# Kernel optimization log

Measured on AMD Instinct MI355X. Metric: run time of the kernel, lower is better.

Reference implementation:

```python
import jax, jax.numpy as jnp
import numpy as np

B, S, E, H = 4, 2048, 1024, 16
D = E // H  # head_dim = 64


def setup_inputs() -> dict:
    key = jax.random.key(0)
    ks = jax.random.split(key, 10)
    scale = 1.0 / np.sqrt(E)
    return {
        "decoder_sequence": jax.random.normal(ks[0], (B, S, E), dtype=jnp.float32),
        # stacked per-head projection weights (math-equivalent to per-head nn.Linear)
        "Wq": jax.random.normal(ks[1], (H, E, D), dtype=jnp.float32) * scale,
        "bq": jnp.zeros((H, D), dtype=jnp.float32),
        "Wk": jax.random.normal(ks[2], (H, E, D), dtype=jnp.float32) * scale,
        "bk": jnp.zeros((H, D), dtype=jnp.float32),
        "Wv": jax.random.normal(ks[3], (H, E, D), dtype=jnp.float32) * scale,
        "bv": jnp.zeros((H, D), dtype=jnp.float32),
        "Wo": jax.random.normal(ks[4], (E, E), dtype=jnp.float32) * scale,
        "bo": jnp.zeros((E,), dtype=jnp.float32),
    }


def reference(decoder_sequence, Wq, bq, Wk, bk, Wv, bv, Wo, bo):
    x = decoder_sequence  # [B,S,E]
    # per-head Q/K/V projections, batched over the head axis
    Q = jnp.einsum('bse,hed->bhsd', x, Wq) + bq[:, None, :]
    K = jnp.einsum('bse,hed->bhsd', x, Wk) + bk[:, None, :]
    V = jnp.einsum('bse,hed->bhsd', x, Wv) + bv[:, None, :]
    # scaled scores with causal mask (upper triangle -> -inf)
    A = jnp.einsum('bhid,bhjd->bhij', Q, K) / jnp.sqrt(jnp.float32(D))
    causal = jnp.tril(jnp.ones((S, S), dtype=bool))  # True where allowed
    A = jnp.where(causal, A, -jnp.inf)
    A = jax.nn.softmax(A, axis=-1)
    Hout = jnp.einsum('bhij,bhjd->bhid', A, V)  # [B,H,S,D]
    # concat heads: [B,S,H*D]
    concat = jnp.transpose(Hout, (0, 2, 1, 3)).reshape(B, S, H * D)
    return concat @ Wo.T + bo
```

## Files before the change

### kernel.cpp

```cpp
#include <hip/hip_runtime.h>
#include <stdint.h>
#include <stddef.h>

typedef __bf16 bf16;
typedef __bf16 bf16x8 __attribute__((ext_vector_type(8)));
typedef __bf16 bf16x4 __attribute__((ext_vector_type(4)));
typedef float  f32x4  __attribute__((ext_vector_type(4)));
typedef float  f32x16 __attribute__((ext_vector_type(16)));
typedef unsigned short ush;
typedef ush ush8 __attribute__((ext_vector_type(8)));
typedef unsigned int uint;

#define B_  4
#define S_  2048
#define E_  1024
#define H_  16
#define D_  64
#define M_  (B_*S_)
#define K_  E_
#define QSCALE 0.18033688011112042f

__device__ __forceinline__ void gload_lds16(const void* g, void* l) {
  __builtin_amdgcn_global_load_lds((const __attribute__((address_space(1))) void*)g,
                                   (__attribute__((address_space(3))) void*)l, 16, 0, 0);
}
__device__ __forceinline__ f32x4 mfma16(bf16x8 a, bf16x8 b, f32x4 c) {
  return __builtin_amdgcn_mfma_f32_16x16x32_bf16(a, b, c, 0, 0, 0);
}
__device__ __forceinline__ f32x16 mfma32(bf16x8 a, bf16x8 b, f32x16 c) {
  return __builtin_amdgcn_mfma_f32_32x32x16_bf16(a, b, c, 0, 0, 0);
}
__device__ __forceinline__ int swz4(int row, int ch) { return ch ^ ((row >> 1) & 3); }
__device__ __forceinline__ uint cvtpk(float lo, float hi) {
  uint r;
  asm("v_cvt_pk_bf16_f32 %0, %1, %2" : "=v"(r) : "v"(lo), "v"(hi));
  return r;
}

__global__ void cast_f32_bf16(const float* __restrict__ src, bf16* __restrict__ dst, int n4) {
  int idx = blockIdx.x * blockDim.x + threadIdx.x;
  int stride = gridDim.x * blockDim.x;
  for (int i = idx; i < n4; i += stride) {
    float4 v = ((const float4*)src)[i];
    union { bf16 b[4]; ushort4 u; } cv;
    cv.b[0] = (bf16)v.x; cv.b[1] = (bf16)v.y; cv.b[2] = (bf16)v.z; cv.b[3] = (bf16)v.w;
    ((ushort4*)dst)[i] = cv.u;
  }
}

__global__ void pack_w_t(const float* __restrict__ Wq, const float* __restrict__ Wk,
                         const float* __restrict__ Wv, bf16* __restrict__ Wp) {
  __shared__ float t[64][65];
  const int tid = threadIdx.x;
  const int wh = blockIdx.y;
  const int which = wh >> 4, h = wh & 15;
  const int e0 = blockIdx.x << 6;
  const float* src = (which == 0) ? Wq : (which == 1 ? Wk : Wv);
  src += (size_t)h * (E_ * D_);
  #pragma unroll
  for (int i = 0; i < 4; ++i) {
    int fi = tid + 256 * i;
    int e = fi >> 4, c = fi & 15;
    float4 v = *(const float4*)(src + (size_t)(e0 + e) * D_ + c * 4);
    t[c * 4 + 0][e] = v.x; t[c * 4 + 1][e] = v.y;
    t[c * 4 + 2][e] = v.z; t[c * 4 + 3][e] = v.w;
  }
  __syncthreads();
  #pragma unroll
  for (int i = 0; i < 2; ++i) {
    int cid = tid + 256 * i;
    int d = cid >> 3, cc = cid & 7;
    ush8 o;
    #pragma unroll
    for (int j = 0; j < 8; ++j) {
      union { bf16 b; ush u; } cv; cv.b = (bf16)t[d][cc * 8 + j]; o[j] = cv.u;
    }
    *(ush8*)(Wp + ((size_t)which * 1024 + h * 64 + d) * K_ + e0 + cc * 8) = o;
  }
}

template <int MODE>
__launch_bounds__(256, 3)
__global__ void gemm_kernel(const bf16* __restrict__ A, const bf16* __restrict__ Bm,
                            int Ntot,
                            const float* __restrict__ bias0, const float* __restrict__ bias1,
                            const float* __restrict__ bias2,
                            bf16* __restrict__ Qo, bf16* __restrict__ Ko, bf16* __restrict__ Vto,
                            float* __restrict__ Fo) {
  __shared__ __align__(16) bf16 lds_a[2][128 * 32];
  __shared__ __align__(16) bf16 lds_b[2][128 * 32];
  const int tid = threadIdx.x;
  const int lane = tid & 63;
  const int w = tid >> 6;
  const int wr = w >> 1, wc = w & 1;
  const int nblk = Ntot >> 7;
  const int qch = gridDim.x >> 3;
  const int swz = (blockIdx.x & 7) * qch + (blockIdx.x >> 3);
  const int mt = swz / nblk, nt = swz % nblk;
  const int m0 = mt << 7, n0 = nt << 7;

  f32x4 acc[4][4] = {};

  auto stage = [&](int buf, int kt) {
    #pragma unroll
    for (int i = 0; i < 2; ++i) {
      int cb = (w * 2 + i) * 64;
      int cid = cb + lane;
      int row = cid >> 2, cir = cid & 3;
      int lch = swz4(row, cir);
      const bf16* ga = A  + (size_t)(m0 + row) * K_ + kt * 32 + lch * 8;
      const bf16* gb = Bm + (size_t)(n0 + row) * K_ + kt * 32 + lch * 8;
      gload_lds16(ga, &lds_a[buf][cb * 8]);
      gload_lds16(gb, &lds_b[buf][cb * 8]);
    }
  };

  const int NT = K_ / 32;
  stage(0, 0);
  for (int kt = 0; kt < NT; ++kt) {
    if (kt + 1 < NT) stage((kt + 1) & 1, kt + 1);
    __syncthreads();
    const bf16x8* pa = (const bf16x8*)&lds_a[kt & 1][0];
    const bf16x8* pb = (const bf16x8*)&lds_b[kt & 1][0];
    bf16x8 af[4], bfr[4];
    #pragma unroll
    for (int mb = 0; mb < 4; ++mb) {
      int row = wr * 64 + mb * 16 + (lane & 15);
      af[mb] = pa[row * 4 + swz4(row, lane >> 4)];
    }
    #pragma unroll
    for (int nb = 0; nb < 4; ++nb) {
      int row = wc * 64 + nb * 16 + (lane & 15);
      bfr[nb] = pb[row * 4 + swz4(row, lane >> 4)];
    }
    #pragma unroll
    for (int mb = 0; mb < 4; ++mb)
      #pragma unroll
      for (int nb = 0; nb < 4; ++nb)
        acc[mb][nb] = mfma16(af[mb], bfr[nb], acc[mb][nb]);
    __syncthreads();
  }

  #pragma unroll
  for (int mb = 0; mb < 4; ++mb) {
    #pragma unroll
    for (int nb = 0; nb < 4; ++nb) {
      const int ni  = n0 + wc * 64 + nb * 16 + (lane & 15);
      const int mi0 = m0 + wr * 64 + mb * 16 + (lane >> 4) * 4;
      if (MODE == 0) {
        const int which = ni >> 10;
        const int col = ni & 1023;
        const float* bp = (which == 0) ? bias0 : (which == 1 ? bias1 : bias2);
        const float bv = bp[col];
        const int hh = col >> 6, d = col & 63;
        const int b = mi0 >> 11, s0r = mi0 & 2047;
        if (which == 2) {
          bf16x4 st;
          #pragma unroll
          for (int r = 0; r < 4; ++r) st[r] = (bf16)(acc[mb][nb][r] + bv);
          *(bf16x4*)(Vto + ((size_t)((b * H_ + hh) * D_ + d)) * S_ + s0r) = st;
        } else {
          bf16* dst = (which == 0) ? Qo : Ko;
          const float sc = (which == 0) ? QSCALE : 1.f;
          #pragma unroll
          for (int r = 0; r < 4; ++r)
            dst[(((size_t)(b * H_ + hh)) * S_ + (s0r + r)) * D_ + d] =
                (bf16)((acc[mb][nb][r] + bv) * sc);
        }
      } else {
        #pragma unroll
        for (int r = 0; r < 4; ++r)
          Fo[(size_t)(mi0 + r) * E_ + ni] = acc[mb][nb][r] + bias0[ni];
      }
    }
  }
}

struct QTile {
  bf16x8 qf[4];
  f32x16 oacc[2];
  float m, l;
};

__device__ __forceinline__ void init_q(QTile& S, const bf16* qrow, int hi) {
  #pragma unroll
  for (int kc = 0; kc < 4; ++kc)
    S.qf[kc] = *(const bf16x8*)(qrow + (2 * kc + hi) * 8);
  #pragma unroll
  for (int r = 0; r < 16; ++r) { S.oacc[0][r] = 0.f; S.oacc[1][r] = 0.f; }
  S.m = -1e30f; S.l = 0.f;
}

__device__ __forceinline__ void tile_step(QTile& S, const bf16* klds, const bf16* vlds,
                                          int sub, int kv0, int qb_, int qg_, int hi, int ln) {
  if (kv0 > qb_ + 31) return;
  const bf16* kbase = klds + sub * (64 * 64);
  f32x16 s0 = {}, s1 = {};
  #pragma unroll
  for (int kc = 0; kc < 4; ++kc) {
    int ch = (2 * kc + hi) ^ (ln & 7);
    bf16x8 k0 = *(const bf16x8*)&kbase[ln * 64 + ch * 8];
    bf16x8 k1 = *(const bf16x8*)&kbase[(32 + ln) * 64 + ch * 8];
    s0 = mfma32(k0, S.qf[kc], s0);
    s1 = mfma32(k1, S.qf[kc], s1);
  }
  if (kv0 + 63 > qb_) {
    #pragma unroll
    for (int r = 0; r < 16; ++r) {
      int crow = (r & 3) + 8 * (r >> 2) + 4 * hi;
      if (kv0 + crow > qg_)      s0[r] = -1e30f;
      if (kv0 + 32 + crow > qg_) s1[r] = -1e30f;
    }
  }
  float mt_ = s0[0];
  #pragma unroll
  for (int r = 1; r < 16; ++r) mt_ = fmaxf(mt_, s0[r]);
  #pragma unroll
  for (int r = 0; r < 16; ++r) mt_ = fmaxf(mt_, s1[r]);
  mt_ = fmaxf(mt_, __shfl_xor(mt_, 32, 64));
  bool resc = mt_ > S.m + 8.f;
  float mnew = resc ? mt_ : S.m;
  float alpha = resc ? exp2f(S.m - mnew) : 1.f;
  S.m = mnew;
  float rs = 0.f;
  #pragma unroll
  for (int r = 0; r < 16; ++r) { float p = exp2f(s0[r] - mnew); s0[r] = p; rs += p; }
  #pragma unroll
  for (int r = 0; r < 16; ++r) { float p = exp2f(s1[r] - mnew); s1[r] = p; rs += p; }
  rs += __shfl_xor(rs, 32, 64);
  S.l = S.l * alpha + rs;
  if (__any(resc)) {
    #pragma unroll
    for (int r = 0; r < 16; ++r) { S.oacc[0][r] *= alpha; S.oacc[1][r] *= alpha; }
  }
  bf16x8 pf[4];
  #pragma unroll
  for (int mtl = 0; mtl < 2; ++mtl) {
    #pragma unroll
    for (int c = 0; c < 2; ++c) {
      const f32x16& p = mtl ? s1 : s0;
      uint wa = cvtpk(p[8 * c + 0], p[8 * c + 1]);
      uint wb = cvtpk(p[8 * c + 2], p[8 * c + 3]);
      uint wcx = cvtpk(p[8 * c + 4], p[8 * c + 5]);
      uint wd = cvtpk(p[8 * c + 6], p[8 * c + 7]);
      asm("v_permlane32_swap_b32 %0, %1" : "+v"(wa), "+v"(wcx));
      asm("v_permlane32_swap_b32 %0, %1" : "+v"(wb), "+v"(wd));
      union { uint u[4]; bf16x8 v; } cvt;
      cvt.u[0] = wa; cvt.u[1] = wb; cvt.u[2] = wcx; cvt.u[3] = wd;
      pf[mtl * 2 + c] = cvt.v;
    }
  }
  #pragma unroll
  for (int dm = 0; dm < 2; ++dm) {
    #pragma unroll
    for (int ks = 0; ks < 4; ++ks) {
      int row = dm * 32 + ln;
      int cfull = sub * 8 + 2 * ks + hi;
      int ch = cfull ^ (ln & 15);
      bf16x8 vf = *(const bf16x8*)&vlds[row * 128 + ch * 8];
      S.oacc[dm] = mfma32(vf, pf[ks], S.oacc[dm]);
    }
  }
}

__device__ __forceinline__ void store_o(const QTile& S, bf16* orow, int hi) {
  float rinv = 1.f / S.l;
  #pragma unroll
  for (int dm = 0; dm < 2; ++dm) {
    #pragma unroll
    for (int g = 0; g < 4; ++g) {
      bf16x4 st;
      #pragma unroll
      for (int i = 0; i < 4; ++i) st[i] = (bf16)(S.oacc[dm][4 * g + i] * rinv);
      *(bf16x4*)(orow + dm * 32 + g * 8 + hi * 4) = st;
    }
  }
}

__launch_bounds__(256, 2)
__global__ void attn_kernel(const bf16* __restrict__ Q, const bf16* __restrict__ K,
                            const bf16* __restrict__ Vt, bf16* __restrict__ Cc) {
  __shared__ __align__(16) bf16 k_lds[2][128 * 64];
  __shared__ __align__(16) bf16 v_lds[2][64 * 128];
  const int tid = threadIdx.x, lane = tid & 63, w = tid >> 6;
  const int hi = lane >> 5, ln = lane & 31;
  const int bid = blockIdx.x;
  const int bh = bid & 63;
  const int x = bid >> 6;
  const int jta = x, jtb = 15 - x;
  const bf16* Kb = K  + (size_t)bh * (S_ * D_);
  const bf16* Vb = Vt + (size_t)bh * (D_ * S_);
  const int b = bh >> 4, hh = bh & 15;

  auto stage2 = [&](int buf, int ph) {
    const int kv0 = ph << 7;
    #pragma unroll
    for (int i = 0; i < 4; ++i) {
      int cb = (w * 4 + i) * 64;
      int cid = cb + lane;
      int row = cid >> 3, cir = cid & 7;
      int lch = cir ^ (row & 7);
      gload_lds16(Kb + (size_t)(kv0 + row) * D_ + lch * 8, &k_lds[buf][cb * 8]);
      int rowv = cid >> 4, cirv = cid & 15;
      int lchv = cirv ^ (rowv & 15);
      gload_lds16(Vb + (size_t)rowv * S_ + kv0 + lchv * 8, &v_lds[buf][cb * 8]);
    }
  };

  {
    const int qb_ = jta * 128 + w * 32, qg_ = qb_ + ln;
    QTile SA;
    init_q(SA, Q + ((size_t)bh * S_ + qg_) * D_, hi);
    const int nph = x + 1;
    stage2(0, 0);
    __syncthreads();
    for (int ph = 0; ph < nph; ++ph) {
      int cur = ph & 1;
      if (ph + 1 < nph) stage2(cur ^ 1, ph + 1);
      tile_step(SA, k_lds[cur], v_lds[cur], 0, ph * 128,      qb_, qg_, hi, ln);
      tile_step(SA, k_lds[cur], v_lds[cur], 1, ph * 128 + 64, qb_, qg_, hi, ln);
      __syncthreads();
    }
    store_o(SA, Cc + ((size_t)(b * S_ + qg_)) * E_ + hh * D_, hi);
  }
  {
    const int qb_ = jtb * 128 + w * 32, qg_ = qb_ + ln;
    QTile SB;
    init_q(SB, Q + ((size_t)bh * S_ + qg_) * D_, hi);
    const int nph = 16 - x;
    stage2(0, 0);
    __syncthreads();
    for (int ph = 0; ph < nph; ++ph) {
      int cur = ph & 1;
      if (ph + 1 < nph) stage2(cur ^ 1, ph + 1);
      tile_step(SB, k_lds[cur], v_lds[cur], 0, ph * 128,      qb_, qg_, hi, ln);
      tile_step(SB, k_lds[cur], v_lds[cur], 1, ph * 128 + 64, qb_, qg_, hi, ln);
      __syncthreads();
    }
    store_o(SB, Cc + ((size_t)(b * S_ + qg_)) * E_ + hh * D_, hi);
  }
}

extern "C" void kernel_launch(void* const* d_in, const int* in_sizes, int n_in,
                              void* d_out, int out_size, void* d_ws, size_t ws_size,
                              hipStream_t stream) {
  const float* x  = (const float*)d_in[0];
  const float* Wq = (const float*)d_in[1];
  const float* bq = (const float*)d_in[2];
  const float* Wk = (const float*)d_in[3];
  const float* bk = (const float*)d_in[4];
  const float* Wv = (const float*)d_in[5];
  const float* bv = (const float*)d_in[6];
  const float* Wo = (const float*)d_in[7];
  const float* bo = (const float*)d_in[8];
  float* out = (float*)d_out;

  uint8_t* ws = (uint8_t*)d_ws;
  bf16* Xbf   = (bf16*)(ws + 0);
  bf16* Wpack = (bf16*)(ws + 16777216);
  bf16* Wot   = (bf16*)(ws + 23068672);
  bf16* Qb    = (bf16*)(ws + 25165824);
  bf16* Kb    = (bf16*)(ws + 41943040);
  bf16* Vtb   = (bf16*)(ws + 75497472);
  bf16* Cc    = Xbf;

  cast_f32_bf16<<<2048, 256, 0, stream>>>(x,  Xbf, (M_ * K_) / 4);
  cast_f32_bf16<<<1024, 256, 0, stream>>>(Wo, Wot, (E_ * E_) / 4);
  pack_w_t<<<dim3(16, 48), 256, 0, stream>>>(Wq, Wk, Wv, Wpack);

  gemm_kernel<0><<<dim3(64 * 24), 256, 0, stream>>>(Xbf, Wpack, 3072, bq, bk, bv,
                                                    Qb, Kb, Vtb, nullptr);

  attn_kernel<<<dim3(512), 256, 0, stream>>>(Qb, Kb, Vtb, Cc);

  gemm_kernel<1><<<dim3(64 * 8), 256, 0, stream>>>(Cc, Wot, 1024, bo, nullptr, nullptr,
                                                   nullptr, nullptr, nullptr, out);
}
```

Before: 189.3 us.

## Compute softmax row sums via MFMA, tree-reduce max, and reswizzle K LDS

The running row-sum of probabilities is now computed with an extra MFMA against a ones vector, using the bf16-rounded P, rather than 32 scalar adds plus a cross-lane shuffle. The max reduction is restructured as a pairwise tree to shorten the dependency chain, and the alpha rescale of l moves inside the rare rescale branch. The K-tile LDS swizzle adds a second XOR term on row bits 3-4 to reduce bank conflicts on the QK fragment reads. This adds four MFMAs per tile and makes the sum use bf16-rounded probabilities, which slightly changes numerics.

```diff
diff --git a/kernel.cpp b/kernel.cpp
--- a/kernel.cpp
+++ b/kernel.cpp
@@ -196,9 +196,10 @@
   if (kv0 > qb_ + 31) return;
   const bf16* kbase = klds + sub * (64 * 64);
   f32x16 s0 = {}, s1 = {};
+  const int lxor = (ln & 7) ^ ((ln >> 3) & 3);
   #pragma unroll
   for (int kc = 0; kc < 4; ++kc) {
-    int ch = (2 * kc + hi) ^ (ln & 7);
+    int ch = (2 * kc + hi) ^ lxor;
     bf16x8 k0 = *(const bf16x8*)&kbase[ln * 64 + ch * 8];
     bf16x8 k1 = *(const bf16x8*)&kbase[(32 + ln) * 64 + ch * 8];
     s0 = mfma32(k0, S.qf[kc], s0);
@@ -212,24 +213,23 @@
       if (kv0 + 32 + crow > qg_) s1[r] = -1e30f;
     }
   }
-  float mt_ = s0[0];
-  #pragma unroll
-  for (int r = 1; r < 16; ++r) mt_ = fmaxf(mt_, s0[r]);
-  #pragma unroll
-  for (int r = 0; r < 16; ++r) mt_ = fmaxf(mt_, s1[r]);
-  mt_ = fmaxf(mt_, __shfl_xor(mt_, 32, 64));
+  float tm[16];
+  #pragma unroll
+  for (int r = 0; r < 16; ++r) tm[r] = fmaxf(s0[r], s1[r]);
+  #pragma unroll
+  for (int st = 8; st >= 1; st >>= 1)
+    #pragma unroll
+    for (int r = 0; r < st; ++r) tm[r] = fmaxf(tm[r], tm[r + st]);
+  float mt_ = fmaxf(tm[0], __shfl_xor(tm[0], 32, 64));
   bool resc = mt_ > S.m + 8.f;
+  float mold = S.m;
   float mnew = resc ? mt_ : S.m;
-  float alpha = resc ? exp2f(S.m - mnew) : 1.f;
   S.m = mnew;
-  float rs = 0.f;
-  #pragma unroll
-  for (int r = 0; r < 16; ++r) { float p = exp2f(s0[r] - mnew); s0[r] = p; rs += p; }
-  #pragma unroll
-  for (int r = 0; r < 16; ++r) { float p = exp2f(s1[r] - mnew); s1[r] = p; rs += p; }
-  rs += __shfl_xor(rs, 32, 64);
-  S.l = S.l * alpha + rs;
+  #pragma unroll
+  for (int r = 0; r < 16; ++r) { s0[r] = exp2f(s0[r] - mnew); s1[r] = exp2f(s1[r] - mnew); }
   if (__any(resc)) {
+    float alpha = resc ? exp2f(mold - mnew) : 1.f;
+    S.l *= alpha;
     #pragma unroll
     for (int r = 0; r < 16; ++r) { S.oacc[0][r] *= alpha; S.oacc[1][r] *= alpha; }
   }
@@ -250,6 +250,11 @@
       pf[mtl * 2 + c] = cvt.v;
     }
   }
+  const bf16 one_ = (bf16)1.f;
+  const bf16x8 vones = {one_, one_, one_, one_, one_, one_, one_, one_};
+  f32x16 lt = {};
+  #pragma unroll
+  for (int ks = 0; ks < 4; ++ks) lt = mfma32(vones, pf[ks], lt);
   #pragma unroll
   for (int dm = 0; dm < 2; ++dm) {
     #pragma unroll
@@ -261,6 +266,7 @@
       S.oacc[dm] = mfma32(vf, pf[ks], S.oacc[dm]);
     }
   }
+  S.l += lt[0];
 }
 
 __device__ __forceinline__ void store_o(const QTile& S, bf16* orow, int hi) {
@@ -299,7 +305,7 @@
       int cb = (w * 4 + i) * 64;
       int cid = cb + lane;
       int row = cid >> 3, cir = cid & 7;
-      int lch = cir ^ (row & 7);
+      int lch = cir ^ (row & 7) ^ ((row >> 3) & 3);
       gload_lds16(Kb + (size_t)(kv0 + row) * D_ + lch * 8, &k_lds[buf][cb * 8]);
       int rowv = cid >> 4, cirv = cid & 15;
       int lchv = cirv ^ (rowv & 15);
```

Result: no change. 189.6 us (+0.2%).
